# Kernel optimization log

Measured on AMD Instinct MI355X. Metric: run time of the kernel, lower is better.

## Reference

```python
import jax, jax.numpy as jnp
import numpy as np

B, T, D, E, H = 8, 2048, 1024, 8, 256
LN_EPS = 1e-5  # torch.nn.LayerNorm default


def setup_inputs() -> dict:
    key = jax.random.key(0)
    ks = jax.random.split(key, 4)
    return {
        "x": jax.random.normal(ks[0], (B, T, D), dtype=jnp.float32),
        "Wg": jax.random.normal(ks[1], (E, D), dtype=jnp.float32) * 0.02,
        "ln_scale": jnp.ones((E, D), dtype=jnp.float32),
        "ln_bias": jnp.zeros((E, D), dtype=jnp.float32),
        "W1": jax.random.normal(ks[2], (E, D, H), dtype=jnp.float32) * 0.02,
        "b1": jnp.zeros((E, H), dtype=jnp.float32),
        "W2": jax.random.normal(ks[3], (E, H, D), dtype=jnp.float32) * 0.02,
        "b2": jnp.zeros((E, D), dtype=jnp.float32),
    }


def reference(x, Wg, ln_scale, ln_bias, W1, b1, W2, b2):
    Bs, Ts, Ds = x.shape
    xt = x.reshape(Bs * Ts, Ds)                      # [N, D]
    logits = xt @ Wg.T                               # [N, E]
    # softmax is monotone, so argmax(softmax(logits)) == argmax(logits)
    top1 = jnp.argmax(logits, axis=-1)               # [N] int

    # LayerNorm normalization is expert-independent; compute once.
    mu = jnp.mean(xt, axis=-1, keepdims=True)
    var = jnp.mean(jnp.square(xt - mu), axis=-1, keepdims=True)
    xhat = (xt - mu) * jax.lax.rsqrt(var + LN_EPS)   # [N, D]

    n_experts = Wg.shape[0]

    def body(y, p):
        s_e, b_e, w1, bb1, w2, bb2, eid = p
        h = jax.nn.gelu((xhat * s_e + b_e) @ w1 + bb1, approximate=False)  # [N, H]
        out = h @ w2 + bb2                                                  # [N, D]
        mask = (top1 == eid)[:, None].astype(out.dtype)
        return y + mask * out, None

    y0 = jnp.zeros_like(xt)
    y, _ = jax.lax.scan(
        body, y0, (ln_scale, ln_bias, W1, b1, W2, b2, jnp.arange(n_experts))
    )
    # dropout p=0.0 is identity
    return y.reshape(Bs, Ts, Ds)
```

## Files before the change

kernel.cpp:

```cpp
#include <hip/hip_runtime.h>
#include <math.h>

#define N_TOK 16384
#define D_DIM 1024
#define E_NUM 8
#define H_DIM 256
#define LN_EPS 1e-5f

#define BM 128
#define BN1 64
#define BN2 128
#define BKG 64
#define MAXTILES (N_TOK / BM + E_NUM)
#define MP (MAXTILES * BM)
#define CSTRIDE 16

typedef __attribute__((ext_vector_type(8))) short bf16x8;
typedef __attribute__((ext_vector_type(4))) float f32x4;

__device__ __forceinline__ unsigned short f2bf(float f) {
  union { float f; unsigned u; } cv; cv.f = f;
  unsigned u = cv.u;
  u += 0x7fffu + ((u >> 16) & 1u);
  return (unsigned short)(u >> 16);
}

__device__ __forceinline__ void gl_lds16(const void* g, void* l) {
  __builtin_amdgcn_global_load_lds(
      (const __attribute__((address_space(1))) unsigned int*)g,
      (__attribute__((address_space(3))) unsigned int*)l, 16, 0, 0);
}

__device__ __forceinline__ float gelu_exact_fast(float v) {
  float u = fabsf(v) * 0.70710678118654752f;
  float t = 1.0f / (1.0f + 0.3275911f * u);
  float poly = t * (0.254829592f + t * (-0.284496736f + t * (1.421413741f
             + t * (-1.453152027f + t * 1.061405429f))));
  float er = 1.0f - poly * __expf(-u * u);
  er = v >= 0.0f ? er : -er;
  return 0.5f * v * (1.0f + er);
}

template <int CTRL>
__device__ __forceinline__ int dppi(int x) {
  return __builtin_amdgcn_update_dpp(0, x, CTRL, 0xf, 0xf, true);
}
template <int CTRL>
__device__ __forceinline__ double dppd(double x) {
  union { double d; int i[2]; } u; u.d = x;
  u.i[0] = dppi<CTRL>(u.i[0]);
  u.i[1] = dppi<CTRL>(u.i[1]);
  return u.d;
}
template <int CTRL>
__device__ __forceinline__ float dppf(float x) {
  union { float f; int i; } u; u.f = x;
  u.i = dppi<CTRL>(u.i);
  return u.f;
}
template <int IMM>
__device__ __forceinline__ double swzd(double x) {
  union { double d; int i[2]; } u; u.d = x;
  u.i[0] = __builtin_amdgcn_ds_swizzle(u.i[0], IMM);
  u.i[1] = __builtin_amdgcn_ds_swizzle(u.i[1], IMM);
  return u.d;
}
template <int IMM>
__device__ __forceinline__ float swzf(float x) {
  union { float f; int i; } u; u.f = x;
  u.i = __builtin_amdgcn_ds_swizzle(u.i, IMM);
  return u.f;
}

__global__ __launch_bounds__(256) void smoe_gate(
    const float* __restrict__ x, const float* __restrict__ wg,
    const float* __restrict__ ln_s, const float* __restrict__ ln_b,
    unsigned short* __restrict__ xhat, int* __restrict__ eid)
{
  int lane = threadIdx.x & 63, wave = threadIdx.x >> 6;
  int t = blockIdx.x * 4 + wave;

  const float4* x4 = (const float4*)x + (size_t)t * 256;
  float4 v[4];
  float s = 0.f, ss = 0.f;
#pragma unroll
  for (int j = 0; j < 4; j++) {
    v[j] = x4[lane + 64 * j];
    s  += v[j].x + v[j].y + v[j].z + v[j].w;
    ss += v[j].x * v[j].x + v[j].y * v[j].y + v[j].z * v[j].z + v[j].w * v[j].w;
  }
  const float4* wg4 = (const float4*)wg;
  double lg[E_NUM];
#pragma unroll
  for (int e = 0; e < E_NUM; e++) {
    double acc = 0.0;
#pragma unroll
    for (int j = 0; j < 4; j++) {
      float4 w = wg4[e * 256 + lane + 64 * j];
      acc += (double)v[j].x * w.x + (double)v[j].y * w.y
           + (double)v[j].z * w.z + (double)v[j].w * w.w;
    }
    lg[e] = acc;
  }

  double a0, a1, a2, a3;
  {
    double p0 = dppd<0xB1>(lg[0]), p1 = dppd<0xB1>(lg[1]);
    double p2 = dppd<0xB1>(lg[2]), p3 = dppd<0xB1>(lg[3]);
    double p4 = dppd<0xB1>(lg[4]), p5 = dppd<0xB1>(lg[5]);
    double p6 = dppd<0xB1>(lg[6]), p7 = dppd<0xB1>(lg[7]);
    bool b = lane & 1;
    a0 = b ? lg[1] + p1 : lg[0] + p0;
    a1 = b ? lg[3] + p3 : lg[2] + p2;
    a2 = b ? lg[5] + p5 : lg[4] + p4;
    a3 = b ? lg[7] + p7 : lg[6] + p6;
  }
  double c0, c1;
  {
    double q0 = dppd<0x4E>(a0), q1 = dppd<0x4E>(a1);
    double q2 = dppd<0x4E>(a2), q3 = dppd<0x4E>(a3);
    bool b = (lane >> 1) & 1;
    c0 = b ? a1 + q1 : a0 + q0;
    c1 = b ? a3 + q3 : a2 + q2;
  }
  double c;
  {
    double r0 = swzd<0x101F>(c0), r1 = swzd<0x101F>(c1);
    bool b = (lane >> 2) & 1;
    c = b ? c1 + r1 : c0 + r0;
  }
  c += dppd<0x128>(c);
  c += swzd<0x401F>(c);
  c += __shfl_xor(c, 32, 64);

  double val = c; int idx = lane & 7;
  {
    double ov = dppd<0xB1>(val); int oi = dppi<0xB1>(idx);
    if (ov > val || (ov == val && oi < idx)) { val = ov; idx = oi; }
  }
  {
    double ov = dppd<0x4E>(val); int oi = dppi<0x4E>(idx);
    if (ov > val || (ov == val && oi < idx)) { val = ov; idx = oi; }
  }
  {
    double ov = dppd<0x124>(val); int oi = dppi<0x124>(idx);
    if (ov > val || (ov == val && oi < idx)) { val = ov; idx = oi; }
  }
  int best = idx;

  s += dppf<0xB1>(s);   ss += dppf<0xB1>(ss);
  s += dppf<0x4E>(s);   ss += dppf<0x4E>(ss);
  s += dppf<0x141>(s);  ss += dppf<0x141>(ss);
  s += dppf<0x128>(s);  ss += dppf<0x128>(ss);
  s += swzf<0x401F>(s); ss += swzf<0x401F>(ss);
  s += __shfl_xor(s, 32, 64);
  ss += __shfl_xor(ss, 32, 64);

  float mean = s * (1.0f / (float)D_DIM);
  float var  = ss * (1.0f / (float)D_DIM) - mean * mean;
  float rstd = 1.0f / sqrtf(var + LN_EPS);

  if (lane == 0) eid[t] = best;

  const float4* s4 = (const float4*)(ln_s + (size_t)best * D_DIM);
  const float4* b4 = (const float4*)(ln_b + (size_t)best * D_DIM);
  ushort4* xo = (ushort4*)(xhat + (size_t)t * D_DIM);
#pragma unroll
  for (int j = 0; j < 4; j++) {
    float4 sc = s4[lane + 64 * j], bi = b4[lane + 64 * j];
    ushort4 o;
    o.x = f2bf((v[j].x - mean) * rstd * sc.x + bi.x);
    o.y = f2bf((v[j].y - mean) * rstd * sc.y + bi.y);
    o.z = f2bf((v[j].z - mean) * rstd * sc.z + bi.z);
    o.w = f2bf((v[j].w - mean) * rstd * sc.w + bi.w);
    xo[lane + 64 * j] = o;
  }
}

__global__ __launch_bounds__(256) void smoe_scatter_cvt(
    const int* __restrict__ eid, int* __restrict__ cnt, int* __restrict__ tokp,
    const float* __restrict__ w1, unsigned short* __restrict__ w1t,
    const float* __restrict__ w2, unsigned short* __restrict__ w2t)
{
  if (blockIdx.x < 64) {
    int t = blockIdx.x * 256 + threadIdx.x;
    int lane = threadIdx.x & 63;
    int e = eid[t];
    int pos = 0;
#pragma unroll
    for (int k = 0; k < E_NUM; k++) {
      bool me = (e == k);
      unsigned long long m = __ballot(me);
      if (m == 0ull) continue;
      int leader = __ffsll((unsigned long long)m) - 1;
      int cw = __popcll(m);
      int base = 0;
      if (lane == leader) base = atomicAdd(&cnt[k * CSTRIDE], cw);
      base = __shfl(base, leader, 64);
      if (me) pos = base + __popcll(m & ((1ull << lane) - 1ull));
    }
    tokp[e * N_TOK + pos] = t;
    return;
  }

  int bid = blockIdx.x - 64;
  const float* in; unsigned short* out; int R, C;
  if (bid < 512) { in = w1; out = w1t; R = D_DIM; C = H_DIM; }
  else           { in = w2; out = w2t; R = H_DIM; C = D_DIM; bid -= 512; }
  int rt = R / 64, ct = C / 64;
  int e = bid / (rt * ct);
  int rem = bid % (rt * ct);
  int r0 = (rem / ct) * 64, c0 = (rem % ct) * 64;
  __shared__ float tile[64][65];
  int tx = threadIdx.x & 63, ty = threadIdx.x >> 6;
  const float* src = in + (size_t)e * R * C;
#pragma unroll
  for (int i = 0; i < 16; i++)
    tile[ty + 4 * i][tx] = src[(size_t)(r0 + ty + 4 * i) * C + c0 + tx];
  __syncthreads();
  unsigned short* dst = out + (size_t)e * R * C;
#pragma unroll
  for (int i = 0; i < 16; i++)
    dst[(size_t)(c0 + ty + 4 * i) * R + r0 + tx] = f2bf(tile[tx][ty + 4 * i]);
}

__device__ __forceinline__ void tile_map(const int* __restrict__ cnt, int mt,
                                         int& e, int& loc, int& ccnt) {
  int tb = 0; e = 0; loc = -1; ccnt = 0;
#pragma unroll
  for (int k = 0; k < E_NUM; k++) {
    int ck = cnt[k * CSTRIDE];
    int ntk = (ck + BM - 1) >> 7;
    if (mt >= tb && mt < tb + ntk) { e = k; loc = (mt - tb) * BM; ccnt = ck; }
    tb += ntk;
  }
}

__global__ __launch_bounds__(256) void smoe_gemm1(
    const unsigned short* __restrict__ xhat,
    const unsigned short* __restrict__ w1t,
    const float* __restrict__ b1,
    const int* __restrict__ cnt,
    const int* __restrict__ tokp,
    unsigned short* __restrict__ hbuf)
{
  int mt = blockIdx.x;
  int e, loc, ccnt;
  tile_map(cnt, mt, e, loc, ccnt);
  if (loc < 0) return;
  int nt = blockIdx.y;
  int tid = threadIdx.x;
  __shared__ unsigned short As[2][BM * BKG];
  __shared__ unsigned short Bs[2][BN1 * BKG];

  int r8 = tid >> 3;
  int c8 = tid & 7;
  int slot = c8 ^ (r8 & 7);

  const unsigned short* asrc[4];
#pragma unroll
  for (int j = 0; j < 4; j++) {
    int rl = loc + r8 + 32 * j;
    int tok = rl < ccnt ? tokp[e * N_TOK + rl] : 0;
    asrc[j] = xhat + (size_t)tok * D_DIM + slot * 8;
  }
  const unsigned short* bsrc[2];
#pragma unroll
  for (int j = 0; j < 2; j++)
    bsrc[j] = w1t + (size_t)e * H_DIM * D_DIM
            + (size_t)(nt * BN1 + r8 + 32 * j) * D_DIM + slot * 8;

  int wave = tid >> 6, lane = tid & 63;
  int wr = (wave >> 1) * 64;
  int wc = (wave & 1) * 32;
  int qm = lane & 15, quad = lane >> 4;

  int arow[4], brow[2], soff[2];
#pragma unroll
  for (int mi = 0; mi < 4; mi++) arow[mi] = (wr + mi * 16 + qm) * BKG;
#pragma unroll
  for (int ni = 0; ni < 2; ni++) brow[ni] = (wc + ni * 16 + qm) * BKG;
#pragma unroll
  for (int kk = 0; kk < 2; kk++) soff[kk] = ((kk * 4 + quad) ^ (qm & 7)) * 8;

  f32x4 acc[4][2] = {};
  int cur = 0;

#pragma unroll
  for (int j = 0; j < 4; j++) gl_lds16(asrc[j], &As[0][j * 2048 + tid * 8]);
#pragma unroll
  for (int j = 0; j < 2; j++) gl_lds16(bsrc[j], &Bs[0][j * 2048 + tid * 8]);
  __syncthreads();

  for (int t = 0; t < D_DIM / BKG; ++t) {
    if (t + 1 < D_DIM / BKG) {
      int k0 = (t + 1) * BKG;
      int nb = cur ^ 1;
#pragma unroll
      for (int j = 0; j < 4; j++) gl_lds16(asrc[j] + k0, &As[nb][j * 2048 + tid * 8]);
#pragma unroll
      for (int j = 0; j < 2; j++) gl_lds16(bsrc[j] + k0, &Bs[nb][j * 2048 + tid * 8]);
    }
    bf16x8 af[2][4], bfr[2][2];
#pragma unroll
    for (int kk = 0; kk < 2; kk++) {
#pragma unroll
      for (int mi = 0; mi < 4; mi++)
        af[kk][mi] = *(const bf16x8*)&As[cur][arow[mi] + soff[kk]];
#pragma unroll
      for (int ni = 0; ni < 2; ni++)
        bfr[kk][ni] = *(const bf16x8*)&Bs[cur][brow[ni] + soff[kk]];
    }
#pragma unroll
    for (int kk = 0; kk < 2; kk++)
#pragma unroll
      for (int mi = 0; mi < 4; mi++)
#pragma unroll
        for (int ni = 0; ni < 2; ni++)
          acc[mi][ni] = __builtin_amdgcn_mfma_f32_16x16x32_bf16(
              af[kk][mi], bfr[kk][ni], acc[mi][ni], 0, 0, 0);
    __syncthreads();
    cur ^= 1;
  }

  int mbase = mt * BM;
#pragma unroll
  for (int ni = 0; ni < 2; ni++) {
    int col = nt * BN1 + wc + ni * 16 + qm;
    float bias = b1[e * H_DIM + col];
#pragma unroll
    for (int mi = 0; mi < 4; mi++) {
      int rl = wr + mi * 16 + quad * 4;
#pragma unroll
      for (int i = 0; i < 4; i++) {
        float g = gelu_exact_fast(acc[mi][ni][i] + bias);
        hbuf[(size_t)(mbase + rl + i) * H_DIM + col] = f2bf(g);
      }
    }
  }
}

__global__ __launch_bounds__(256) void smoe_gemm2(
    const unsigned short* __restrict__ hbuf,
    const unsigned short* __restrict__ w2t,
    const float* __restrict__ b2,
    const int* __restrict__ cnt,
    const int* __restrict__ tokp,
    float* __restrict__ y)
{
  int mt = blockIdx.x;
  int e, loc, ccnt;
  tile_map(cnt, mt, e, loc, ccnt);
  if (loc < 0) return;
  int nt = blockIdx.y;
  int tid = threadIdx.x;
  __shared__ unsigned short As[2][BM * BKG];
  __shared__ unsigned short Bs[2][BN2 * BKG];

  int r8 = tid >> 3;
  int c8 = tid & 7;
  int slot = c8 ^ (r8 & 7);

  const unsigned short* asrc[4];
#pragma unroll
  for (int j = 0; j < 4; j++)
    asrc[j] = hbuf + (size_t)(mt * BM + r8 + 32 * j) * H_DIM + slot * 8;
  const unsigned short* bsrc[4];
#pragma unroll
  for (int j = 0; j < 4; j++)
    bsrc[j] = w2t + (size_t)e * D_DIM * H_DIM
            + (size_t)(nt * BN2 + r8 + 32 * j) * H_DIM + slot * 8;

  int wave = tid >> 6, lane = tid & 63;
  int wr = (wave >> 1) * 64;
  int wc = (wave & 1) * 64;
  int qm = lane & 15, quad = lane >> 4;

  int arow[4], brow[4], soff[2];
#pragma unroll
  for (int mi = 0; mi < 4; mi++) arow[mi] = (wr + mi * 16 + qm) * BKG;
#pragma unroll
  for (int ni = 0; ni < 4; ni++) brow[ni] = (wc + ni * 16 + qm) * BKG;
#pragma unroll
  for (int kk = 0; kk < 2; kk++) soff[kk] = ((kk * 4 + quad) ^ (qm & 7)) * 8;

  f32x4 acc[4][4] = {};
  int cur = 0;

#pragma unroll
  for (int j = 0; j < 4; j++) gl_lds16(asrc[j], &As[0][j * 2048 + tid * 8]);
#pragma unroll
  for (int j = 0; j < 4; j++) gl_lds16(bsrc[j], &Bs[0][j * 2048 + tid * 8]);
  __syncthreads();

  for (int t = 0; t < H_DIM / BKG; ++t) {
    if (t + 1 < H_DIM / BKG) {
      int k0 = (t + 1) * BKG;
      int nb = cur ^ 1;
#pragma unroll
      for (int j = 0; j < 4; j++) gl_lds16(asrc[j] + k0, &As[nb][j * 2048 + tid * 8]);
#pragma unroll
      for (int j = 0; j < 4; j++) gl_lds16(bsrc[j] + k0, &Bs[nb][j * 2048 + tid * 8]);
    }
    bf16x8 af[2][4], bfr[2][4];
#pragma unroll
    for (int kk = 0; kk < 2; kk++) {
#pragma unroll
      for (int mi = 0; mi < 4; mi++)
        af[kk][mi] = *(const bf16x8*)&As[cur][arow[mi] + soff[kk]];
#pragma unroll
      for (int ni = 0; ni < 4; ni++)
        bfr[kk][ni] = *(const bf16x8*)&Bs[cur][brow[ni] + soff[kk]];
    }
#pragma unroll
    for (int kk = 0; kk < 2; kk++)
#pragma unroll
      for (int mi = 0; mi < 4; mi++)
#pragma unroll
        for (int ni = 0; ni < 4; ni++)
          acc[mi][ni] = __builtin_amdgcn_mfma_f32_16x16x32_bf16(
              af[kk][mi], bfr[kk][ni], acc[mi][ni], 0, 0, 0);
    __syncthreads();
    cur ^= 1;
  }

#pragma unroll
  for (int mi = 0; mi < 4; mi++) {
#pragma unroll
    for (int i = 0; i < 4; i++) {
      int rl = loc + wr + mi * 16 + quad * 4 + i;
      if (rl >= ccnt) continue;
      int tok = tokp[e * N_TOK + rl];
#pragma unroll
      for (int ni = 0; ni < 4; ni++) {
        int col = nt * BN2 + wc + ni * 16 + qm;
        y[(size_t)tok * D_DIM + col] = acc[mi][ni][i] + b2[e * D_DIM + col];
      }
    }
  }
}

extern "C" void kernel_launch(void* const* d_in, const int* in_sizes, int n_in,
                              void* d_out, int out_size, void* d_ws, size_t ws_size,
                              hipStream_t stream) {
  (void)in_sizes; (void)n_in; (void)out_size; (void)ws_size;
  const float* x    = (const float*)d_in[0];
  const float* wg   = (const float*)d_in[1];
  const float* ln_s = (const float*)d_in[2];
  const float* ln_b = (const float*)d_in[3];
  const float* w1   = (const float*)d_in[4];
  const float* b1   = (const float*)d_in[5];
  const float* w2   = (const float*)d_in[6];
  const float* b2   = (const float*)d_in[7];
  float* y = (float*)d_out;

  char* ws = (char*)d_ws;
  size_t off = 0;
  auto alloc = [&](size_t bytes) {
    void* p = ws + off;
    off = (off + bytes + 255) & ~(size_t)255;
    return p;
  };
  unsigned short* xhat = (unsigned short*)alloc((size_t)N_TOK * D_DIM * 2);
  unsigned short* w1t  = (unsigned short*)alloc((size_t)E_NUM * D_DIM * H_DIM * 2);
  unsigned short* w2t  = (unsigned short*)alloc((size_t)E_NUM * D_DIM * H_DIM * 2);
  unsigned short* hbuf = (unsigned short*)alloc((size_t)MP * H_DIM * 2);
  int* eid    = (int*)alloc((size_t)N_TOK * 4);
  int* tokp   = (int*)alloc((size_t)E_NUM * N_TOK * 4);
  int* cnt    = (int*)alloc((size_t)E_NUM * CSTRIDE * 4);

  hipMemsetAsync(cnt, 0, (size_t)E_NUM * CSTRIDE * 4, stream);
  smoe_gate<<<N_TOK / 4, 256, 0, stream>>>(x, wg, ln_s, ln_b, xhat, eid);
  smoe_scatter_cvt<<<64 + 1024, 256, 0, stream>>>(eid, cnt, tokp, w1, w1t, w2, w2t);
  smoe_gemm1<<<dim3(MAXTILES, H_DIM / BN1), 256, 0, stream>>>(xhat, w1t, b1, cnt, tokp, hbuf);
  smoe_gemm2<<<dim3(MAXTILES, D_DIM / BN2), 256, 0, stream>>>(hbuf, w2t, b2, cnt, tokp, y);
}
```

Baseline: 218.1 us.

## Fuse token scatter into gate kernel and widen GEMM1 N tile

The gate kernel now appends each token to its expert list with one atomic per token, which removes the separate eid buffer and the ballot-based scatter stage from the conversion kernel. The weight-conversion kernel becomes standalone. Separately, GEMM1's N tile is doubled so each wave computes a 64x64 block with 16 accumulators. This halves the grid along H and raises register use. The per-token atomics may contend on eight counters and leave tokens within each expert in nondeterministic order.

```diff
diff --git a/kernel.cpp b/kernel.cpp
--- a/kernel.cpp
+++ b/kernel.cpp
@@ -8,7 +8,7 @@
 #define LN_EPS 1e-5f
 
 #define BM 128
-#define BN1 64
+#define BN1 128
 #define BN2 128
 #define BKG 64
 #define MAXTILES (N_TOK / BM + E_NUM)
@@ -75,7 +75,8 @@
 __global__ __launch_bounds__(256) void smoe_gate(
     const float* __restrict__ x, const float* __restrict__ wg,
     const float* __restrict__ ln_s, const float* __restrict__ ln_b,
-    unsigned short* __restrict__ xhat, int* __restrict__ eid)
+    unsigned short* __restrict__ xhat,
+    int* __restrict__ cnt, int* __restrict__ tokp)
 {
   int lane = threadIdx.x & 63, wave = threadIdx.x >> 6;
   int t = blockIdx.x * 4 + wave;
@@ -160,8 +161,6 @@
   float var  = ss * (1.0f / (float)D_DIM) - mean * mean;
   float rstd = 1.0f / sqrtf(var + LN_EPS);
 
-  if (lane == 0) eid[t] = best;
-
   const float4* s4 = (const float4*)(ln_s + (size_t)best * D_DIM);
   const float4* b4 = (const float4*)(ln_b + (size_t)best * D_DIM);
   ushort4* xo = (ushort4*)(xhat + (size_t)t * D_DIM);
@@ -175,35 +174,18 @@
     o.w = f2bf((v[j].w - mean) * rstd * sc.w + bi.w);
     xo[lane + 64 * j] = o;
   }
-}
-
-__global__ __launch_bounds__(256) void smoe_scatter_cvt(
-    const int* __restrict__ eid, int* __restrict__ cnt, int* __restrict__ tokp,
+
+  if (lane == 0) {
+    int pos = atomicAdd(&cnt[best * CSTRIDE], 1);
+    tokp[best * N_TOK + pos] = t;
+  }
+}
+
+__global__ __launch_bounds__(256) void smoe_cvt(
     const float* __restrict__ w1, unsigned short* __restrict__ w1t,
     const float* __restrict__ w2, unsigned short* __restrict__ w2t)
 {
-  if (blockIdx.x < 64) {
-    int t = blockIdx.x * 256 + threadIdx.x;
-    int lane = threadIdx.x & 63;
-    int e = eid[t];
-    int pos = 0;
-#pragma unroll
-    for (int k = 0; k < E_NUM; k++) {
-      bool me = (e == k);
-      unsigned long long m = __ballot(me);
-      if (m == 0ull) continue;
-      int leader = __ffsll((unsigned long long)m) - 1;
-      int cw = __popcll(m);
-      int base = 0;
-      if (lane == leader) base = atomicAdd(&cnt[k * CSTRIDE], cw);
-      base = __shfl(base, leader, 64);
-      if (me) pos = base + __popcll(m & ((1ull << lane) - 1ull));
-    }
-    tokp[e * N_TOK + pos] = t;
-    return;
-  }
-
-  int bid = blockIdx.x - 64;
+  int bid = blockIdx.x;
   const float* in; unsigned short* out; int R, C;
   if (bid < 512) { in = w1; out = w1t; R = D_DIM; C = H_DIM; }
   else           { in = w2; out = w2t; R = H_DIM; C = D_DIM; bid -= 512; }
@@ -264,32 +246,32 @@
     int tok = rl < ccnt ? tokp[e * N_TOK + rl] : 0;
     asrc[j] = xhat + (size_t)tok * D_DIM + slot * 8;
   }
-  const unsigned short* bsrc[2];
-#pragma unroll
-  for (int j = 0; j < 2; j++)
+  const unsigned short* bsrc[4];
+#pragma unroll
+  for (int j = 0; j < 4; j++)
     bsrc[j] = w1t + (size_t)e * H_DIM * D_DIM
             + (size_t)(nt * BN1 + r8 + 32 * j) * D_DIM + slot * 8;
 
   int wave = tid >> 6, lane = tid & 63;
   int wr = (wave >> 1) * 64;
-  int wc = (wave & 1) * 32;
+  int wc = (wave & 1) * 64;
   int qm = lane & 15, quad = lane >> 4;
 
-  int arow[4], brow[2], soff[2];
+  int arow[4], brow[4], soff[2];
 #pragma unroll
   for (int mi = 0; mi < 4; mi++) arow[mi] = (wr + mi * 16 + qm) * BKG;
 #pragma unroll
-  for (int ni = 0; ni < 2; ni++) brow[ni] = (wc + ni * 16 + qm) * BKG;
+  for (int ni = 0; ni < 4; ni++) brow[ni] = (wc + ni * 16 + qm) * BKG;
 #pragma unroll
   for (int kk = 0; kk < 2; kk++) soff[kk] = ((kk * 4 + quad) ^ (qm & 7)) * 8;
 
-  f32x4 acc[4][2] = {};
+  f32x4 acc[4][4] = {};
   int cur = 0;
 
 #pragma unroll
   for (int j = 0; j < 4; j++) gl_lds16(asrc[j], &As[0][j * 2048 + tid * 8]);
 #pragma unroll
-  for (int j = 0; j < 2; j++) gl_lds16(bsrc[j], &Bs[0][j * 2048 + tid * 8]);
+  for (int j = 0; j < 4; j++) gl_lds16(bsrc[j], &Bs[0][j * 2048 + tid * 8]);
   __syncthreads();
 
   for (int t = 0; t < D_DIM / BKG; ++t) {
@@ -299,16 +281,16 @@
 #pragma unroll
       for (int j = 0; j < 4; j++) gl_lds16(asrc[j] + k0, &As[nb][j * 2048 + tid * 8]);
 #pragma unroll
-      for (int j = 0; j < 2; j++) gl_lds16(bsrc[j] + k0, &Bs[nb][j * 2048 + tid * 8]);
-    }
-    bf16x8 af[2][4], bfr[2][2];
+      for (int j = 0; j < 4; j++) gl_lds16(bsrc[j] + k0, &Bs[nb][j * 2048 + tid * 8]);
+    }
+    bf16x8 af[2][4], bfr[2][4];
 #pragma unroll
     for (int kk = 0; kk < 2; kk++) {
 #pragma unroll
       for (int mi = 0; mi < 4; mi++)
         af[kk][mi] = *(const bf16x8*)&As[cur][arow[mi] + soff[kk]];
 #pragma unroll
-      for (int ni = 0; ni < 2; ni++)
+      for (int ni = 0; ni < 4; ni++)
         bfr[kk][ni] = *(const bf16x8*)&Bs[cur][brow[ni] + soff[kk]];
     }
 #pragma unroll
@@ -316,7 +298,7 @@
 #pragma unroll
       for (int mi = 0; mi < 4; mi++)
 #pragma unroll
-        for (int ni = 0; ni < 2; ni++)
+        for (int ni = 0; ni < 4; ni++)
           acc[mi][ni] = __builtin_amdgcn_mfma_f32_16x16x32_bf16(
               af[kk][mi], bfr[kk][ni], acc[mi][ni], 0, 0, 0);
     __syncthreads();
@@ -325,7 +307,7 @@
 
   int mbase = mt * BM;
 #pragma unroll
-  for (int ni = 0; ni < 2; ni++) {
+  for (int ni = 0; ni < 4; ni++) {
     int col = nt * BN1 + wc + ni * 16 + qm;
     float bias = b1[e * H_DIM + col];
 #pragma unroll
@@ -465,13 +447,12 @@
   unsigned short* w1t  = (unsigned short*)alloc((size_t)E_NUM * D_DIM * H_DIM * 2);
   unsigned short* w2t  = (unsigned short*)alloc((size_t)E_NUM * D_DIM * H_DIM * 2);
   unsigned short* hbuf = (unsigned short*)alloc((size_t)MP * H_DIM * 2);
-  int* eid    = (int*)alloc((size_t)N_TOK * 4);
   int* tokp   = (int*)alloc((size_t)E_NUM * N_TOK * 4);
   int* cnt    = (int*)alloc((size_t)E_NUM * CSTRIDE * 4);
 
   hipMemsetAsync(cnt, 0, (size_t)E_NUM * CSTRIDE * 4, stream);
-  smoe_gate<<<N_TOK / 4, 256, 0, stream>>>(x, wg, ln_s, ln_b, xhat, eid);
-  smoe_scatter_cvt<<<64 + 1024, 256, 0, stream>>>(eid, cnt, tokp, w1, w1t, w2, w2t);
+  smoe_gate<<<N_TOK / 4, 256, 0, stream>>>(x, wg, ln_s, ln_b, xhat, cnt, tokp);
+  smoe_cvt<<<1024, 256, 0, stream>>>(w1, w1t, w2, w2t);
   smoe_gemm1<<<dim3(MAXTILES, H_DIM / BN1), 256, 0, stream>>>(xhat, w1t, b1, cnt, tokp, hbuf);
   smoe_gemm2<<<dim3(MAXTILES, D_DIM / BN2), 256, 0, stream>>>(hbuf, w2t, b2, cnt, tokp, y);
 }
```

New measurement: 225.0 us. 1.03x slower.
